# Kernel tuning notes

Measured on AMD Instinct MI355X. Metric: run time of the kernel, lower is better.

## Reference

```python
import jax, jax.numpy as jnp
import numpy as np

B, CD, NF, V, D = 16384, 13, 26, 100000, 64
BOT = [256, 128]
TOP = [512, 256, 128]
NUM_EMB = NF + 1            # 27 (bottom output + 26 categorical)
NUM_INTER = NUM_EMB * (NUM_EMB - 1) // 2  # 351
TOP_IN = NUM_INTER + NUM_EMB * D          # 2079
BN_INV = 1.0 / np.sqrt(1.0 + 1e-5)        # eval-mode BatchNorm: running_mean=0, running_var=1


def _lin(key, fan_in, fan_out):
    kw, kb = jax.random.split(key)
    s = 1.0 / np.sqrt(fan_in)
    W = jax.random.uniform(kw, (fan_in, fan_out), minval=-s, maxval=s, dtype=jnp.float32)
    b = jax.random.uniform(kb, (fan_out,), minval=-s, maxval=s, dtype=jnp.float32)
    return W, b


def setup_inputs() -> dict:
    key = jax.random.key(0)
    ks = jax.random.split(key, 16)
    continuous = jax.random.normal(ks[0], (B, CD), dtype=jnp.float32)
    cat_idx = jax.random.randint(ks[1], (B, NF), 0, V, dtype=jnp.int32)
    emb_tables = jax.random.normal(ks[2], (NF, V, D), dtype=jnp.float32)  # nn.Embedding init ~ N(0,1)
    W1, b1 = _lin(ks[3], CD, BOT[0]);   g1 = jnp.ones((BOT[0],)); be1 = jnp.zeros((BOT[0],))
    W2, b2 = _lin(ks[4], BOT[0], BOT[1]); g2 = jnp.ones((BOT[1],)); be2 = jnp.zeros((BOT[1],))
    W3, b3 = _lin(ks[5], BOT[1], D)
    W4, b4 = _lin(ks[6], TOP_IN, TOP[0]); g4 = jnp.ones((TOP[0],)); be4 = jnp.zeros((TOP[0],))
    W5, b5 = _lin(ks[7], TOP[0], TOP[1]); g5 = jnp.ones((TOP[1],)); be5 = jnp.zeros((TOP[1],))
    W6, b6 = _lin(ks[8], TOP[1], TOP[2]); g6 = jnp.ones((TOP[2],)); be6 = jnp.zeros((TOP[2],))
    W7, b7 = _lin(ks[9], TOP[2], 1)
    return dict(continuous=continuous, cat_idx=cat_idx, emb_tables=emb_tables,
                W1=W1, b1=b1, g1=g1, be1=be1, W2=W2, b2=b2, g2=g2, be2=be2, W3=W3, b3=b3,
                W4=W4, b4=b4, g4=g4, be4=be4, W5=W5, b5=b5, g5=g5, be5=be5,
                W6=W6, b6=b6, g6=g6, be6=be6, W7=W7, b7=b7)


def _bn(x, g, b):
    # eval-mode BatchNorm1d with running_mean=0, running_var=1
    return g * (x * BN_INV) + b


def reference(continuous, cat_idx, emb_tables,
              W1, b1, g1, be1, W2, b2, g2, be2, W3, b3,
              W4, b4, g4, be4, W5, b5, g5, be5, W6, b6, g6, be6, W7, b7):
    # Bottom MLP: 13 -> 256 -> 128 -> 64
    h = jax.nn.relu(_bn(continuous @ W1 + b1, g1, be1))
    h = jax.nn.relu(_bn(h @ W2 + b2, g2, be2))
    bottom = h @ W3 + b3                         # [B, D]

    # Embedding gather: one table per categorical feature
    emb = emb_tables[jnp.arange(NF), cat_idx]    # [B, NF, D]
    all_emb = jnp.concatenate([bottom[:, None, :], emb], axis=1)  # [B, 27, D]

    # Pairwise dot-product interactions via one bmm + triu gather
    Z = jnp.einsum('bnd,bmd->bnm', all_emb, all_emb)              # [B, 27, 27]
    iu, ju = np.triu_indices(NUM_EMB, k=1)                        # row-major i<j (matches torch loop order)
    inter = Z[:, iu, ju]                                          # [B, 351]

    top_in = jnp.concatenate([inter, all_emb.reshape(all_emb.shape[0], -1)], axis=1)  # [B, 2079]

    # Top MLP: 2079 -> 512 -> 256 -> 128 -> 1
    t = jax.nn.relu(_bn(top_in @ W4 + b4, g4, be4))
    t = jax.nn.relu(_bn(t @ W5 + b5, g5, be5))
    t = jax.nn.relu(_bn(t @ W6 + b6, g6, be6))
    scores = t @ W7 + b7                                          # [B, 1]
    return scores
```

## Files before the change

kernel.cpp:

```cpp
#include <hip/hip_runtime.h>
#include <stdint.h>
#include <stddef.h>

#define BATCH   16384
#define CDIM    13
#define NFEAT   26
#define VROWS   100000
#define EDIM    64
#define NEMB    27
#define NINTER  351
#define TOPIN   2079
#define KP4     2112
#define BN_INVF 0.9999950000374997f

typedef __attribute__((ext_vector_type(8)))  __bf16 bf16x8;
typedef __attribute__((ext_vector_type(4)))  float  f32x4;
typedef __attribute__((ext_vector_type(16))) float  f32x16;
typedef __attribute__((ext_vector_type(4)))  uint32_t uint4v;

__device__ __forceinline__ uint32_t f2bf(float f){
  uint32_t u = __float_as_uint(f);
  return (u + 0x7fffu + ((u >> 16) & 1u)) >> 16;
}
__device__ __forceinline__ float bf2f(uint32_t h){ return __uint_as_float(h << 16); }
__device__ __forceinline__ uint32_t pack2(float a, float b){
  return f2bf(a) | (f2bf(b) << 16);
}
__device__ __forceinline__ void async_load16(const void* g, void* l){
  __builtin_amdgcn_global_load_lds(
      (const __attribute__((address_space(1))) uint32_t*)g,
      (__attribute__((address_space(3))) uint32_t*)l, 16, 0, 0);
}
__device__ __forceinline__ int rswz(int row){ return ((row ^ (row >> 3)) & 7) << 3; }

__device__ __forceinline__ void transpose_tile(
    float (*tile)[65], const float* __restrict__ src, unsigned short* __restrict__ dst,
    int K, int N, int Kpad, int remap, int kb, int nb){
  int k0 = kb*64, n0 = nb*64, t = threadIdx.x;
  int srcBase = remap ? ((k0 < 1728) ? (k0 + 351) : (k0 - 1728)) : k0;
  #pragma unroll 4
  for(int p = 0; p < 16; p++){
    int kr = p*4 + (t >> 6), nc = t & 63;
    float v = 0.f;
    if(k0 + kr < K && (n0 + nc) < N) v = src[(size_t)(srcBase + kr) * N + n0 + nc];
    tile[kr][nc] = v;
  }
  __syncthreads();
  #pragma unroll 4
  for(int p = 0; p < 16; p++){
    int nr = p*4 + (t >> 6), kc = t & 63;
    if(k0 + kc < Kpad && (n0 + nr) < N)
      dst[(size_t)(n0 + nr) * Kpad + k0 + kc] = (unsigned short)f2bf(tile[kc][nr]);
  }
}

__global__ __launch_bounds__(256) void prep(
    const float* __restrict__ cont,
    const float* __restrict__ W1, const float* __restrict__ W2, const float* __restrict__ W3,
    const float* __restrict__ W4, const float* __restrict__ W5, const float* __restrict__ W6,
    unsigned short* __restrict__ xphi, unsigned short* __restrict__ xplo,
    unsigned short* __restrict__ W1t, unsigned short* __restrict__ W2t,
    unsigned short* __restrict__ W3t, unsigned short* __restrict__ W4t,
    unsigned short* __restrict__ W5t, unsigned short* __restrict__ W6t){
  __shared__ float tile[64][65];
  int bid = blockIdx.x;
  if(bid < 264){ transpose_tile(tile, W4, W4t, TOPIN, 512, KP4, 1, bid % 33, bid / 33); }
  else if(bid < 296){ int r = bid-264; transpose_tile(tile, W5, W5t, 512, 256, 512, 0, r % 8, r / 8); }
  else if(bid < 304){ int r = bid-296; transpose_tile(tile, W6, W6t, 256, 128, 256, 0, r % 4, r / 4); }
  else if(bid < 312){ int r = bid-304; transpose_tile(tile, W2, W2t, 256, 128, 256, 0, r % 4, r / 4); }
  else if(bid < 314){ int r = bid-312; transpose_tile(tile, W3, W3t, 128, 64, 128, 0, r, 0); }
  else if(bid < 318){ int r = bid-314; transpose_tile(tile, W1, W1t, CDIM, 256, 32, 0, 0, r); }
  else {
    int row = (bid - 318) * 256 + threadIdx.x;
    const float* xr = cont + (size_t)row * CDIM;
    uint32_t uh[16], ul[16];
    #pragma unroll
    for(int k = 0; k < 16; k++){
      uint32_t h0=0, h1=0, l0=0, l1=0;
      if(2*k < CDIM){
        float x = xr[2*k]; h0 = f2bf(x); l0 = f2bf(x - bf2f(h0));
      }
      if(2*k+1 < CDIM){
        float x = xr[2*k+1]; h1 = f2bf(x); l1 = f2bf(x - bf2f(h1));
      }
      uh[k] = h0 | (h1 << 16);
      ul[k] = l0 | (l1 << 16);
    }
    #pragma unroll
    for(int s = 0; s < 4; s++){
      uint4v vh, vl;
      #pragma unroll
      for(int e = 0; e < 4; e++){ vh[e] = uh[4*s+e]; vl[e] = ul[4*s+e]; }
      *(uint4v*)(xphi + (size_t)row*32 + s*8) = vh;
      *(uint4v*)(xplo + (size_t)row*32 + s*8) = vl;
    }
  }
}

__global__ __launch_bounds__(256) void bottom_mfma(
    const unsigned short* __restrict__ xphi, const unsigned short* __restrict__ xplo,
    const unsigned short* __restrict__ W1t, const unsigned short* __restrict__ W2t,
    const unsigned short* __restrict__ W3t,
    const float* __restrict__ b1, const float* __restrict__ g1, const float* __restrict__ be1,
    const float* __restrict__ b2, const float* __restrict__ g2, const float* __restrict__ be2,
    const float* __restrict__ b3,
    unsigned short* __restrict__ bottomBF){
  __shared__ unsigned short h1hi[64*256];
  __shared__ unsigned short h1lo[64*256];
  __shared__ unsigned short h2hi[64*128];
  __shared__ unsigned short h2lo[64*128];
  int t = threadIdx.x, w = t >> 6, l = t & 63;
  int m0 = blockIdx.x * 64;
  int lr = l & 15, lk = (l >> 4) * 8;

  {
    bf16x8 axh[4], axl[4];
    #pragma unroll
    for(int mt = 0; mt < 4; mt++){
      size_t ro = (size_t)(m0 + mt*16 + lr) * 32 + lk;
      axh[mt] = *(const bf16x8*)(xphi + ro);
      axl[mt] = *(const bf16x8*)(xplo + ro);
    }
    #pragma unroll
    for(int nt = 0; nt < 4; nt++){
      int n = (w*4 + nt)*16 + lr;
      bf16x8 bw = *(const bf16x8*)(W1t + (size_t)n*32 + lk);
      f32x4 acc[4];
      #pragma unroll
      for(int mt = 0; mt < 4; mt++){
        #pragma unroll
        for(int e = 0; e < 4; e++) acc[mt][e] = 0.f;
        acc[mt] = __builtin_amdgcn_mfma_f32_16x16x32_bf16(axh[mt], bw, acc[mt], 0, 0, 0);
        acc[mt] = __builtin_amdgcn_mfma_f32_16x16x32_bf16(axl[mt], bw, acc[mt], 0, 0, 0);
      }
      float sc = g1[n]*BN_INVF, bo = be1[n], bi = b1[n];
      #pragma unroll
      for(int mt = 0; mt < 4; mt++){
        #pragma unroll
        for(int q = 0; q < 4; q++){
          int row = mt*16 + (l >> 4)*4 + q;
          float y = fmaxf(sc*(acc[mt][q] + bi) + bo, 0.f);
          uint32_t hb = f2bf(y);
          int idx = row*256 + (n ^ rswz(row));
          h1hi[idx] = (unsigned short)hb;
          h1lo[idx] = (unsigned short)f2bf(y - bf2f(hb));
        }
      }
    }
  }
  __syncthreads();

  {
    f32x4 acc[4][2];
    #pragma unroll
    for(int mt = 0; mt < 4; mt++)
      #pragma unroll
      for(int nt = 0; nt < 2; nt++)
        #pragma unroll
        for(int e = 0; e < 4; e++) acc[mt][nt][e] = 0.f;
    for(int ks = 0; ks < 8; ks++){
      bf16x8 bw[2];
      #pragma unroll
      for(int nt = 0; nt < 2; nt++){
        int n = (w*2 + nt)*16 + lr;
        bw[nt] = *(const bf16x8*)(W2t + (size_t)n*256 + ks*32 + lk);
      }
      #pragma unroll
      for(int mt = 0; mt < 4; mt++){
        int row = mt*16 + lr;
        int idx = row*256 + ((ks*32 + lk) ^ rswz(row));
        bf16x8 ah = *(const bf16x8*)(h1hi + idx);
        bf16x8 al = *(const bf16x8*)(h1lo + idx);
        #pragma unroll
        for(int nt = 0; nt < 2; nt++){
          acc[mt][nt] = __builtin_amdgcn_mfma_f32_16x16x32_bf16(ah, bw[nt], acc[mt][nt], 0, 0, 0);
          acc[mt][nt] = __builtin_amdgcn_mfma_f32_16x16x32_bf16(al, bw[nt], acc[mt][nt], 0, 0, 0);
        }
      }
    }
    #pragma unroll
    for(int nt = 0; nt < 2; nt++){
      int n = (w*2 + nt)*16 + lr;
      float sc = g2[n]*BN_INVF, bo = be2[n], bi = b2[n];
      #pragma unroll
      for(int mt = 0; mt < 4; mt++){
        #pragma unroll
        for(int q = 0; q < 4; q++){
          int row = mt*16 + (l >> 4)*4 + q;
          float y = fmaxf(sc*(acc[mt][nt][q] + bi) + bo, 0.f);
          uint32_t hb = f2bf(y);
          int idx = row*128 + (n ^ rswz(row));
          h2hi[idx] = (unsigned short)hb;
          h2lo[idx] = (unsigned short)f2bf(y - bf2f(hb));
        }
      }
    }
  }
  __syncthreads();

  {
    f32x4 acc[4];
    #pragma unroll
    for(int mt = 0; mt < 4; mt++)
      #pragma unroll
      for(int e = 0; e < 4; e++) acc[mt][e] = 0.f;
    int n = w*16 + lr;
    for(int ks = 0; ks < 4; ks++){
      bf16x8 bw = *(const bf16x8*)(W3t + (size_t)n*128 + ks*32 + lk);
      #pragma unroll
      for(int mt = 0; mt < 4; mt++){
        int row = mt*16 + lr;
        int idx = row*128 + ((ks*32 + lk) ^ rswz(row));
        bf16x8 ah = *(const bf16x8*)(h2hi + idx);
        bf16x8 al = *(const bf16x8*)(h2lo + idx);
        acc[mt] = __builtin_amdgcn_mfma_f32_16x16x32_bf16(ah, bw, acc[mt], 0, 0, 0);
        acc[mt] = __builtin_amdgcn_mfma_f32_16x16x32_bf16(al, bw, acc[mt], 0, 0, 0);
      }
    }
    float bi = b3[n];
    #pragma unroll
    for(int mt = 0; mt < 4; mt++){
      #pragma unroll
      for(int q = 0; q < 4; q++){
        int row = m0 + mt*16 + (l >> 4)*4 + q;
        bottomBF[(size_t)row*64 + n] = (unsigned short)f2bf(acc[mt][q] + bi);
      }
    }
  }
}

__global__ __launch_bounds__(256) void interact(
    const unsigned short* __restrict__ bottomBF, const int* __restrict__ cat_idx,
    const float* __restrict__ emb, unsigned short* __restrict__ top_in){
  __shared__ unsigned short inter_s[4][352];
  int w = threadIdx.x >> 6, l = threadIdx.x & 63;
  int b = blockIdx.x * 4 + w;
  int r = l & 31, h = l >> 5;
  bool active = (r < NEMB);
  uint4v q[4];
  if(active && r == 0){
    const unsigned short* sb = bottomBF + (size_t)b * 64;
    #pragma unroll
    for(int s = 0; s < 4; s++) q[s] = *(const uint4v*)(sb + h*8 + s*16);
  } else if(active){
    int f = r - 1;
    int idx = cat_idx[b * NFEAT + f];
    const float* src = emb + ((size_t)f * VROWS + (size_t)idx) * 64;
    #pragma unroll
    for(int s = 0; s < 4; s++){
      int k0 = h*8 + s*16;
      float4 v0 = *(const float4*)(src + k0);
      float4 v1 = *(const float4*)(src + k0 + 4);
      q[s][0] = pack2(v0.x, v0.y); q[s][1] = pack2(v0.z, v0.w);
      q[s][2] = pack2(v1.x, v1.y); q[s][3] = pack2(v1.z, v1.w);
    }
  } else {
    #pragma unroll
    for(int s = 0; s < 4; s++){ q[s][0]=0; q[s][1]=0; q[s][2]=0; q[s][3]=0; }
  }
  if(active){
    #pragma unroll
    for(int s = 0; s < 4; s++)
      *(uint4v*)(top_in + (size_t)b*KP4 + r*64 + h*8 + s*16) = q[s];
  }
  f32x16 acc;
  #pragma unroll
  for(int i = 0; i < 16; i++) acc[i] = 0.f;
  #pragma unroll
  for(int s = 0; s < 4; s++){
    bf16x8 a = __builtin_bit_cast(bf16x8, q[s]);
    acc = __builtin_amdgcn_mfma_f32_32x32x16_bf16(a, a, acc, 0, 0, 0);
  }
  if(active){
    #pragma unroll
    for(int qq = 0; qq < 16; qq++){
      int i = (qq & 3) + 8*(qq >> 2) + 4*h;
      if(i < r){
        int p = i*(53 - i)/2 + (r - i - 1);
        inter_s[w][p] = (unsigned short)f2bf(acc[qq]);
      }
    }
  }
  __syncthreads();
  size_t basei = (size_t)b*KP4 + 1728;
  for(int t0 = l; t0 < 176; t0 += 64){
    uint32_t lo = inter_s[w][2*t0];
    uint32_t hi = (2*t0 + 1 < NINTER) ? (uint32_t)inter_s[w][2*t0 + 1] : 0u;
    *(uint32_t*)(top_in + basei + 2*t0) = lo | (hi << 16);
  }
  if(l < 16) *(uint32_t*)(top_in + (size_t)b*KP4 + 2080 + 2*l) = 0;
}

template<int KSTEPS, int NB, bool FUSE>
__global__ __launch_bounds__(256) void gemm_top(
    const unsigned short* __restrict__ A, int sA,
    const unsigned short* __restrict__ Bw, int sB,
    const float* __restrict__ bias, const float* __restrict__ gg,
    const float* __restrict__ be,
    unsigned short* __restrict__ out, int sOut,
    const float* __restrict__ W7, const float* __restrict__ b7,
    float* __restrict__ scores){
  __shared__ unsigned short As[128*64];
  __shared__ unsigned short Bs[128*64];
  __shared__ float h6s[FUSE ? 128*132 : 1];
  __shared__ float w7s[FUSE ? 128 : 1];
  int nwg = gridDim.x;
  int bid = blockIdx.x;
  int lin = (bid & 7) * (nwg >> 3) + (bid >> 3);
  int m0 = (lin / NB) * 128, n0 = (lin % NB) * 128;
  int t = threadIdx.x, w = t >> 6, l = t & 63;
  int wr = (w >> 1) * 64, wc = (w & 1) * 64;
  f32x4 acc[4][4];
  #pragma unroll
  for(int i = 0; i < 4; i++)
    #pragma unroll
    for(int j = 0; j < 4; j++)
      #pragma unroll
      for(int e = 0; e < 4; e++) acc[i][j][e] = 0.f;

  const unsigned short* gA[4];
  const unsigned short* gB[4];
  char* ldsA[4];
  char* ldsB[4];
  #pragma unroll
  for(int i = 0; i < 4; i++){
    int o   = w*4096 + i*1024 + l*16;
    int row = o >> 7;
    int cb  = (o & 127) ^ ((row & 7) << 4);
    gA[i] = A  + (size_t)(m0 + row)*sA + (cb >> 1);
    gB[i] = Bw + (size_t)(n0 + row)*sB + (cb >> 1);
    ldsA[i] = (char*)As + o;
    ldsB[i] = (char*)Bs + o;
  }
  int lr = l & 15;
  int rs = (l & 7) << 4;
  int o1 = ((l >> 4) * 16) ^ rs;

  for(int kt = 0; kt < KSTEPS; kt++){
    #pragma unroll
    for(int i = 0; i < 4; i++){
      async_load16(gA[i] + kt*64, ldsA[i]);
      async_load16(gB[i] + kt*64, ldsB[i]);
    }
    __syncthreads();
    #pragma unroll
    for(int ks = 0; ks < 2; ks++){
      int ko = o1 ^ (ks << 6);
      bf16x8 af[4], bfr[4];
      #pragma unroll
      for(int x = 0; x < 4; x++){
        af[x]  = *(const bf16x8*)((const char*)As + (wr + x*16 + lr)*128 + ko);
        bfr[x] = *(const bf16x8*)((const char*)Bs + (wc + x*16 + lr)*128 + ko);
      }
      #pragma unroll
      for(int tr = 0; tr < 4; tr++)
        #pragma unroll
        for(int tc = 0; tc < 4; tc++)
          acc[tr][tc] = __builtin_amdgcn_mfma_f32_16x16x32_bf16(af[tr], bfr[tc], acc[tr][tc], 0, 0, 0);
    }
    __syncthreads();
  }

  if constexpr(!FUSE){
    #pragma unroll
    for(int tc = 0; tc < 4; tc++){
      int n = n0 + wc + tc*16 + lr;
      float sc = gg[n]*BN_INVF, bo = be[n], bi = bias[n];
      #pragma unroll
      for(int tr = 0; tr < 4; tr++){
        int mb = m0 + wr + tr*16 + (l >> 4)*4;
        #pragma unroll
        for(int qq = 0; qq < 4; qq++){
          float y = fmaxf(sc*(acc[tr][tc][qq] + bi) + bo, 0.f);
          out[(size_t)(mb + qq)*sOut + n] = (unsigned short)f2bf(y);
        }
      }
    }
  } else {
    if(t < 128) w7s[t] = W7[t];
    #pragma unroll
    for(int tc = 0; tc < 4; tc++){
      int n = wc + tc*16 + lr;
      float sc = gg[n0+n]*BN_INVF, bo = be[n0+n], bi = bias[n0+n];
      #pragma unroll
      for(int tr = 0; tr < 4; tr++){
        int mb = wr + tr*16 + (l >> 4)*4;
        #pragma unroll
        for(int qq = 0; qq < 4; qq++)
          h6s[(mb + qq)*132 + n] = fmaxf(sc*(acc[tr][tc][qq] + bi) + bo, 0.f);
      }
    }
    __syncthreads();
    if(t < 128){
      float a7 = b7[0];
      #pragma unroll 8
      for(int c = 0; c < 128; c++) a7 = fmaf(h6s[t*132 + c], w7s[c], a7);
      scores[m0 + t] = a7;
    }
  }
}

static inline size_t alignup(size_t x){ return (x + 255) & ~(size_t)255; }

extern "C" void kernel_launch(void* const* d_in, const int* in_sizes, int n_in,
                              void* d_out, int out_size, void* d_ws, size_t ws_size,
                              hipStream_t stream){
  const float* cont = (const float*)d_in[0];
  const int*   cat  = (const int*)  d_in[1];
  const float* emb  = (const float*)d_in[2];
  const float* W1 = (const float*)d_in[3],  *b1 = (const float*)d_in[4];
  const float* g1 = (const float*)d_in[5],  *be1= (const float*)d_in[6];
  const float* W2 = (const float*)d_in[7],  *b2 = (const float*)d_in[8];
  const float* g2 = (const float*)d_in[9],  *be2= (const float*)d_in[10];
  const float* W3 = (const float*)d_in[11], *b3 = (const float*)d_in[12];
  const float* W4 = (const float*)d_in[13], *b4 = (const float*)d_in[14];
  const float* g4 = (const float*)d_in[15], *be4= (const float*)d_in[16];
  const float* W5 = (const float*)d_in[17], *b5 = (const float*)d_in[18];
  const float* g5 = (const float*)d_in[19], *be5= (const float*)d_in[20];
  const float* W6 = (const float*)d_in[21], *b6 = (const float*)d_in[22];
  const float* g6 = (const float*)d_in[23], *be6= (const float*)d_in[24];
  const float* W7 = (const float*)d_in[25], *b7 = (const float*)d_in[26];

  char* ws = (char*)d_ws;
  unsigned short* bottomBF = (unsigned short*)ws; ws += alignup((size_t)BATCH*64*2);
  unsigned short* xphi = (unsigned short*)ws; ws += alignup((size_t)BATCH*32*2);
  unsigned short* xplo = (unsigned short*)ws; ws += alignup((size_t)BATCH*32*2);
  unsigned short* W1t  = (unsigned short*)ws; ws += alignup((size_t)256*32*2);
  unsigned short* W2t  = (unsigned short*)ws; ws += alignup((size_t)128*256*2);
  unsigned short* W3t  = (unsigned short*)ws; ws += alignup((size_t)64*128*2);
  unsigned short* topi = (unsigned short*)ws; ws += alignup((size_t)BATCH*KP4*2);
  unsigned short* W4t  = (unsigned short*)ws; ws += alignup((size_t)512*KP4*2);
  unsigned short* W5t  = (unsigned short*)ws; ws += alignup((size_t)256*512*2);
  unsigned short* W6t  = (unsigned short*)ws; ws += alignup((size_t)128*256*2);
  unsigned short* h4   = (unsigned short*)ws; ws += alignup((size_t)BATCH*512*2);
  unsigned short* h5   = (unsigned short*)ws; ws += alignup((size_t)BATCH*256*2);
  (void)ws_size; (void)n_in; (void)in_sizes; (void)out_size;

  hipLaunchKernelGGL(prep, dim3(382), dim3(256), 0, stream,
                     cont, W1, W2, W3, W4, W5, W6,
                     xphi, xplo, W1t, W2t, W3t, W4t, W5t, W6t);
  hipLaunchKernelGGL(bottom_mfma, dim3(BATCH/64), dim3(256), 0, stream,
                     xphi, xplo, W1t, W2t, W3t,
                     b1, g1, be1, b2, g2, be2, b3, bottomBF);
  hipLaunchKernelGGL(interact, dim3(BATCH/4), dim3(256), 0, stream, bottomBF, cat, emb, topi);
  hipLaunchKernelGGL((gemm_top<33, 4, false>), dim3(512), dim3(256), 0, stream,
                     topi, KP4, W4t, KP4, b4, g4, be4, h4, 512,
                     (const float*)nullptr, (const float*)nullptr, (float*)nullptr);
  hipLaunchKernelGGL((gemm_top<8, 2, false>), dim3(256), dim3(256), 0, stream,
                     h4, 512, W5t, 512, b5, g5, be5, h5, 256,
                     (const float*)nullptr, (const float*)nullptr, (float*)nullptr);
  hipLaunchKernelGGL((gemm_top<4, 1, true>), dim3(128), dim3(256), 0, stream,
                     h5, 256, W6t, 256, b6, g6, be6, (unsigned short*)nullptr, 0,
                     W7, b7, (float*)d_out);
}
```

Baseline: 125.2 us.

## Add triple-buffered 256x128 tile GEMM kernel for the first top-MLP layer

Replaces the single-buffered 128x128 gemm_top used for the 2079->512 layer with a new gemm_deep kernel. It uses 512-thread blocks, 256x128 output tiles, and a three-stage LDS ring of async global-to-LDS loads that prefetches two K-steps ahead, synchronised with vmcnt waits and raised wave priority around the MFMA block. The goal is to hide global load latency behind MFMA work and to reuse each B tile across more rows. The cost is 144 KB of LDS per block, which limits occupancy, and only 256 blocks in the grid.

```diff
diff --git a/kernel.cpp b/kernel.cpp
--- a/kernel.cpp
+++ b/kernel.cpp
@@ -291,6 +291,102 @@
   if(l < 16) *(uint32_t*)(top_in + (size_t)b*KP4 + 2080 + 2*l) = 0;
 }
 
+template<int KSTEPS, int NB>
+__global__ __launch_bounds__(512, 2) void gemm_deep(
+    const unsigned short* __restrict__ A, int sA,
+    const unsigned short* __restrict__ Bw, int sB,
+    const float* __restrict__ bias, const float* __restrict__ gg,
+    const float* __restrict__ be,
+    unsigned short* __restrict__ out, int sOut){
+  __shared__ char smem[3*49152];
+  int nwg = gridDim.x;
+  int bid = blockIdx.x;
+  int lin = (bid & 7) * (nwg >> 3) + (bid >> 3);
+  int m0 = (lin / NB) * 256, n0 = (lin % NB) * 128;
+  int t = threadIdx.x, w = t >> 6, l = t & 63;
+  int wr = (w >> 1) * 64, wc = (w & 1) * 64;
+  f32x4 acc[4][4];
+  #pragma unroll
+  for(int i = 0; i < 4; i++)
+    #pragma unroll
+    for(int j = 0; j < 4; j++)
+      #pragma unroll
+      for(int e = 0; e < 4; e++) acc[i][j][e] = 0.f;
+
+  const unsigned short* g[6];
+  int ldsOff[6];
+  #pragma unroll
+  for(int i = 0; i < 6; i++){
+    if(i < 4){
+      int o = i*8192 + t*16;
+      int row = o >> 7;
+      int cb  = (o & 127) ^ ((row & 7) << 4);
+      g[i] = A + (size_t)(m0 + row)*sA + (cb >> 1);
+      ldsOff[i] = o;
+    } else {
+      int o = (i-4)*8192 + t*16;
+      int row = o >> 7;
+      int cb  = (o & 127) ^ ((row & 7) << 4);
+      g[i] = Bw + (size_t)(n0 + row)*sB + (cb >> 1);
+      ldsOff[i] = 32768 + o;
+    }
+  }
+  int lr = l & 15;
+  int o1 = ((l >> 4) * 16) ^ ((l & 7) << 4);
+
+  #pragma unroll
+  for(int i = 0; i < 6; i++) async_load16(g[i], smem + ldsOff[i]);
+  #pragma unroll
+  for(int i = 0; i < 6; i++) async_load16(g[i] + 64, smem + 49152 + ldsOff[i]);
+  asm volatile("s_waitcnt vmcnt(6)" ::: "memory");
+  __builtin_amdgcn_s_barrier();
+
+  for(int kt = 0; kt < KSTEPS; kt++){
+    int cur = kt % 3;
+    int nxt2 = (kt + 2) % 3;
+    int ksrc = (kt + 2 < KSTEPS) ? (kt + 2) : (KSTEPS - 1);
+    #pragma unroll
+    for(int i = 0; i < 6; i++)
+      async_load16(g[i] + ksrc*64, smem + nxt2*49152 + ldsOff[i]);
+    const char* bA = smem + cur*49152;
+    const char* bB = bA + 32768;
+    __builtin_amdgcn_s_setprio(1);
+    #pragma unroll
+    for(int ks = 0; ks < 2; ks++){
+      int ko = o1 ^ (ks << 6);
+      bf16x8 af[4], bfr[4];
+      #pragma unroll
+      for(int x = 0; x < 4; x++){
+        af[x]  = *(const bf16x8*)(bA + (wr + x*16 + lr)*128 + ko);
+        bfr[x] = *(const bf16x8*)(bB + (wc + x*16 + lr)*128 + ko);
+      }
+      #pragma unroll
+      for(int tr = 0; tr < 4; tr++)
+        #pragma unroll
+        for(int tc = 0; tc < 4; tc++)
+          acc[tr][tc] = __builtin_amdgcn_mfma_f32_16x16x32_bf16(af[tr], bfr[tc], acc[tr][tc], 0, 0, 0);
+    }
+    __builtin_amdgcn_s_setprio(0);
+    asm volatile("s_waitcnt vmcnt(6)" ::: "memory");
+    __builtin_amdgcn_s_barrier();
+  }
+
+  #pragma unroll
+  for(int tc = 0; tc < 4; tc++){
+    int n = n0 + wc + tc*16 + lr;
+    float sc = gg[n]*BN_INVF, bo = be[n], bi = bias[n];
+    #pragma unroll
+    for(int tr = 0; tr < 4; tr++){
+      int mb = m0 + wr + tr*16 + (l >> 4)*4;
+      #pragma unroll
+      for(int qq = 0; qq < 4; qq++){
+        float y = fmaxf(sc*(acc[tr][tc][qq] + bi) + bo, 0.f);
+        out[(size_t)(mb + qq)*sOut + n] = (unsigned short)f2bf(y);
+      }
+    }
+  }
+}
+
 template<int KSTEPS, int NB, bool FUSE>
 __global__ __launch_bounds__(256) void gemm_top(
     const unsigned short* __restrict__ A, int sA,
@@ -333,8 +429,7 @@
     ldsB[i] = (char*)Bs + o;
   }
   int lr = l & 15;
-  int rs = (l & 7) << 4;
-  int o1 = ((l >> 4) * 16) ^ rs;
+  int o1 = ((l >> 4) * 16) ^ ((l & 7) << 4);
 
   for(int kt = 0; kt < KSTEPS; kt++){
     #pragma unroll
@@ -443,9 +538,8 @@
                      xphi, xplo, W1t, W2t, W3t,
                      b1, g1, be1, b2, g2, be2, b3, bottomBF);
   hipLaunchKernelGGL(interact, dim3(BATCH/4), dim3(256), 0, stream, bottomBF, cat, emb, topi);
-  hipLaunchKernelGGL((gemm_top<33, 4, false>), dim3(512), dim3(256), 0, stream,
-                     topi, KP4, W4t, KP4, b4, g4, be4, h4, 512,
-                     (const float*)nullptr, (const float*)nullptr, (float*)nullptr);
+  hipLaunchKernelGGL((gemm_deep<33, 4>), dim3(256), dim3(512), 0, stream,
+                     topi, KP4, W4t, KP4, b4, g4, be4, h4, 512);
   hipLaunchKernelGGL((gemm_top<8, 2, false>), dim3(256), dim3(256), 0, stream,
                      h4, 512, W5t, 512, b5, g5, be5, h5, 256,
                      (const float*)nullptr, (const float*)nullptr, (float*)nullptr);
```

Result: faster. 119.3 us (-4.7%).
